# Kernel optimization log

Hardware: AMD Instinct MI355X
Metric: run time of the kernel (lower is better)

The kernel has to match this reference:

```python
import jax, jax.numpy as jnp
import numpy as np

D_MODEL = 1024


def pos_encoding(seq_len, d_model):
    # pos: [S,1], i: [d/2]
    pos = jnp.arange(seq_len, dtype=jnp.float32)[:, None]
    i = jnp.arange(0, d_model, 2, dtype=jnp.float32)
    angle_rates = 1.0 / jnp.power(10000.0, i / d_model)
    angle_rads = pos * angle_rates  # [S, d/2]
    # NOTE: original concatenates sin block then cos block (not interleaved)
    return jnp.concatenate([jnp.sin(angle_rads), jnp.cos(angle_rads)], axis=-1)  # [S, d]


def setup_inputs() -> dict:
    key = jax.random.key(0)
    ks = jax.random.split(key, 4)
    B, S, D = 4, 2048, D_MODEL
    scale = 1.0 / np.sqrt(D)
    x = jax.random.normal(ks[0], (B, S, D), dtype=jnp.float32)
    Wq = jax.random.normal(ks[1], (D, D), dtype=jnp.float32) * scale
    Wk = jax.random.normal(ks[2], (D, D), dtype=jnp.float32) * scale
    Wv = jax.random.normal(ks[3], (D, D), dtype=jnp.float32) * scale
    bq = jnp.zeros((D,), dtype=jnp.float32)
    bk = jnp.zeros((D,), dtype=jnp.float32)
    bv = jnp.zeros((D,), dtype=jnp.float32)
    return {"x": x, "Wq": Wq, "bq": bq, "Wk": Wk, "bk": bk, "Wv": Wv, "bv": bv}


def reference(x, Wq, bq, Wk, bk, Wv, bv):
    B, S, D = x.shape
    pe = pos_encoding(S, D)  # [S, D]
    h = x + pe[None, :, :]
    q = jnp.einsum('bsd,de->bse', h, Wq) + bq
    k = jnp.einsum('bsd,de->bse', h, Wk) + bk
    v = jnp.einsum('bsd,de->bse', h, Wv) + bv
    logits = jnp.einsum('bqd,bkd->bqk', q, k) / jnp.sqrt(jnp.float32(D))
    attn = jax.nn.softmax(logits, axis=-1)
    out = jnp.einsum('bqk,bkd->bqd', attn, v)
    return x + out
```

## Files before the change

kernel.cpp:

```cpp
#include <hip/hip_runtime.h>
#include <stdint.h>


#define AS1(p) ((__attribute__((address_space(1))) void*)(p))
#define AS3(p) ((__attribute__((address_space(3))) void*)(p))

typedef _Float16 f16x8 __attribute__((ext_vector_type(8)));
typedef _Float16 f16x4 __attribute__((ext_vector_type(4)));
typedef float f32x4 __attribute__((ext_vector_type(4)));

__global__ __launch_bounds__(256) void prep(const float* __restrict__ x,
                                            _Float16* __restrict__ h,
                                            const float* __restrict__ Wq,
                                            const float* __restrict__ Wk,
                                            const float* __restrict__ Wv,
                                            _Float16* __restrict__ Wt,
                                            float* __restrict__ rowsum) {
  const int bx = blockIdx.x;
  const int tid = threadIdx.x;
  if (bx < 8192) {
    const size_t e = ((size_t)bx * 256 + tid) * 4;
    const int d = (int)(e & 1023);
    const int s = (int)((e >> 10) & 2047);
    const float4 xv = *(const float4*)(x + e);
    const int half = d >> 9;
    const int j0 = d & 511;
    const float c = -0.017988946039016f;
    f16x4 o;
#pragma unroll
    for (int t = 0; t < 4; t++) {
      const float r = __expf((float)(j0 + t) * c);
      const float a = (float)s * r;
      const float p = half ? __cosf(a) : __sinf(a);
      const float xe = (t == 0) ? xv.x : (t == 1) ? xv.y : (t == 2) ? xv.z : xv.w;
      o[t] = (_Float16)(xe + p);
    }
    *(f16x4*)(h + e) = o;
  } else if (bx < 11264) {
    __shared__ float t[32][33];
    const int w = bx - 8192;
    const int z = w >> 10;
    const int rem = w & 1023;
    const int n0 = (rem & 31) * 32, k0 = (rem >> 5) * 32;
    const float* W = (z == 0) ? Wq : (z == 1) ? Wk : Wv;
    _Float16* o = Wt + (size_t)z * 1048576;
    const int tx = tid & 31, ty = tid >> 5;
#pragma unroll
    for (int i = ty; i < 32; i += 8)
      t[i][tx] = W[(size_t)(k0 + i) * 1024 + (n0 + tx)];
    __syncthreads();
#pragma unroll
    for (int i = ty; i < 32; i += 8)
      o[(size_t)(n0 + i) * 1024 + (k0 + tx)] = (_Float16)t[tx][i];
  } else {
    rowsum[(bx - 11264) * 256 + tid] = 0.f;
  }
}

template <int MODE, int NBUF>
__global__ __launch_bounds__(256) void gemm_bt(
    const _Float16* __restrict__ A0, long long sA,
    const _Float16* __restrict__ B0, long long sB,
    void* __restrict__ C0, long long sC,
    const float* __restrict__ aux0, const float* __restrict__ aux1,
    const float* __restrict__ aux2, float* __restrict__ rowsum,
    const _Float16* __restrict__ tin, _Float16* __restrict__ tout,
    long long sX, const int K, const int N, const int ldc) {
  __shared__ __align__(16) _Float16 As[NBUF * 128 * 32];
  __shared__ __align__(16) _Float16 Bs[NBUF * 128 * 32];
  const int tid = threadIdx.x;
  const int bid = blockIdx.x;

  if (MODE == 1 && bid >= 1024) {
    _Float16(*t)[33] = (_Float16(*)[33])As;
    const int w = bid - 1024;
    const int z = w >> 11;
    const int rem = w & 2047;
    const int d0 = (rem & 31) * 32, j0 = (rem >> 5) * 32;
    const _Float16* in = tin + (size_t)z * 2097152;
    _Float16* out = tout + (size_t)z * 2097152;
    const int tx = tid & 31, ty = tid >> 5;
#pragma unroll
    for (int i = ty; i < 32; i += 8)
      t[i][tx] = in[(size_t)(j0 + i) * 1024 + (d0 + tx)];
    __syncthreads();
#pragma unroll
    for (int i = ty; i < 32; i += 8)
      out[(size_t)(d0 + i) * 2048 + (j0 + tx)] = t[tx][i];
    return;
  }

  int z, bm0, bn0;
  if (MODE == 0) {
    const int c = bid & 7, t = bid >> 3;
    const int mhi = t & 7, u = t >> 3;
    bm0 = (mhi * 8 + c) * 128;
    bn0 = (u & 7) * 128;
    z = u >> 3;
  } else if (MODE == 1) {
    const int c = bid & 7, t = bid >> 3;
    const int zx = (t & 7) * 8 + c;
    const int y = t >> 3;
    z = zx >> 4; bm0 = (zx & 15) * 128; bn0 = y * 128;
  } else {
    const int c = bid & 7, t = bid >> 3;
    const int zx = (t & 3) * 8 + c;
    const int y = t >> 2;
    z = zx >> 3; bm0 = (zx & 7) * 128; bn0 = y * 128;
  }
  const _Float16* A = A0 + (size_t)z * sA;
  const _Float16* Bt = B0 + (size_t)z * sB;

  const _Float16* a0 = A + (size_t)(bm0 + (tid >> 2)) * K + (tid & 3) * 8;
  const _Float16* a1 = a0 + (size_t)64 * K;
  const _Float16* b0 = Bt + (size_t)(bn0 + (tid >> 2)) * K + (tid & 3) * 8;
  const _Float16* b1 = b0 + (size_t)64 * K;

  const int lane = tid & 63, wave = tid >> 6;
  const int wr = wave >> 1, wc = wave & 1;
  const int quad = lane >> 4, l16 = lane & 15;

  f32x4 acc[4][4];
#pragma unroll
  for (int i = 0; i < 4; i++)
#pragma unroll
    for (int j = 0; j < 4; j++) {
      f32x4 zz = {0.f, 0.f, 0.f, 0.f};
      acc[i][j] = zz;
    }

  for (int k0 = 0; k0 < K; k0 += 32 * NBUF) {
    __syncthreads();
#pragma unroll
    for (int u = 0; u < NBUF; u++) {
      __builtin_amdgcn_global_load_lds(AS1(a0 + k0 + u * 32),
                                       AS3(&As[u * 4096 + tid * 8]), 16, 0, 0);
      __builtin_amdgcn_global_load_lds(AS1(a1 + k0 + u * 32),
                                       AS3(&As[u * 4096 + tid * 8 + 2048]), 16, 0, 0);
      __builtin_amdgcn_global_load_lds(AS1(b0 + k0 + u * 32),
                                       AS3(&Bs[u * 4096 + tid * 8]), 16, 0, 0);
      __builtin_amdgcn_global_load_lds(AS1(b1 + k0 + u * 32),
                                       AS3(&Bs[u * 4096 + tid * 8 + 2048]), 16, 0, 0);
    }
    __syncthreads();
#pragma unroll
    for (int u = 0; u < NBUF; u++) {
      f16x8 af[4], bfr[4];
#pragma unroll
      for (int i = 0; i < 4; i++)
        af[i] = *(const f16x8*)&As[u * 4096 + (wr * 64 + i * 16 + l16) * 32 + quad * 8];
#pragma unroll
      for (int j = 0; j < 4; j++)
        bfr[j] = *(const f16x8*)&Bs[u * 4096 + (wc * 64 + j * 16 + l16) * 32 + quad * 8];
#pragma unroll
      for (int i = 0; i < 4; i++)
#pragma unroll
        for (int j = 0; j < 4; j++)
          acc[i][j] = __builtin_amdgcn_mfma_f32_16x16x32_f16(af[i], bfr[j],
                                                             acc[i][j], 0, 0, 0);
    }
  }

  const int rowb = bm0 + wr * 64 + quad * 4;
  const int colb = bn0 + wc * 64 + l16;
  if (MODE == 0) {
    _Float16* C = (_Float16*)C0 + (size_t)z * sC;
    const float* bias = (z == 0) ? aux0 : (z == 1) ? aux1 : aux2;
#pragma unroll
    for (int i = 0; i < 4; i++)
#pragma unroll
      for (int j = 0; j < 4; j++) {
        const int gn = colb + j * 16;
        const float bb = bias[gn];
#pragma unroll
        for (int r = 0; r < 4; r++)
          C[(size_t)(rowb + i * 16 + r) * N + gn] = (_Float16)(acc[i][j][r] + bb);
      }
  } else if (MODE == 1) {
    _Float16* C = (_Float16*)C0 + (size_t)z * sC;
    float rs[4] = {0.f, 0.f, 0.f, 0.f};
#pragma unroll
    for (int i = 0; i < 4; i++)
#pragma unroll
      for (int j = 0; j < 4; j++) {
        const int gn = colb + j * 16;
        f16x4 o;
        float pj = 0.f;
#pragma unroll
        for (int r = 0; r < 4; r++) {
          const float e = __expf(acc[i][j][r] * 0.03125f);
          o[r] = (_Float16)e;
          pj += e;
        }
        rs[j] += pj;
        *(f16x4*)&C[(size_t)gn * ldc + rowb + i * 16] = o;
      }
#pragma unroll
    for (int j = 0; j < 4; j++) {
      float v = rs[j];
      v += __shfl_xor(v, 16);
      v += __shfl_xor(v, 32);
      if (quad == 0) atomicAdd(&rowsum[z * 2048 + colb + j * 16], v);
    }
  } else {
    float* C = (float*)C0 + (size_t)z * sC;
    const float* X = aux0 + (size_t)z * sX;
    float inv[4];
#pragma unroll
    for (int j = 0; j < 4; j++)
      inv[j] = 1.0f / rowsum[z * 2048 + colb + j * 16];
#pragma unroll
    for (int i = 0; i < 4; i++)
#pragma unroll
      for (int j = 0; j < 4; j++) {
        const int gn = colb + j * 16;
        const size_t base = (size_t)gn * ldc + rowb + i * 16;
        const float4 xv = *(const float4*)(X + base);
        float4 o;
        o.x = acc[i][j][0] * inv[j] + xv.x;
        o.y = acc[i][j][1] * inv[j] + xv.y;
        o.z = acc[i][j][2] * inv[j] + xv.z;
        o.w = acc[i][j][3] * inv[j] + xv.w;
        *(float4*)(C + base) = o;
      }
  }
}

extern "C" void kernel_launch(void* const* d_in, const int* in_sizes, int n_in,
                              void* d_out, int out_size, void* d_ws, size_t ws_size,
                              hipStream_t stream) {
  (void)in_sizes; (void)n_in; (void)out_size; (void)ws_size;
  const float* x  = (const float*)d_in[0];
  const float* Wq = (const float*)d_in[1];
  const float* bq = (const float*)d_in[2];
  const float* Wk = (const float*)d_in[3];
  const float* bk = (const float*)d_in[4];
  const float* Wv = (const float*)d_in[5];
  const float* bv = (const float*)d_in[6];
  float* out = (float*)d_out;
  char* ws = (char*)d_ws;

  _Float16* h    = (_Float16*)(ws);
  _Float16* vT   = (_Float16*)(ws);
  _Float16* Wt   = (_Float16*)(ws + 16777216);
  _Float16* qkv  = (_Float16*)(ws + 23068672);
  _Float16* attn = (_Float16*)(ws + 73400320);
  float* rowsum  = (float*)   (ws + 106954752);

  const long long E = 8388608;

  prep<<<11296, 256, 0, stream>>>(x, h, Wq, Wk, Wv, Wt, rowsum);

  gemm_bt<0, 1><<<1536, 256, 0, stream>>>(
      h, 0LL, Wt, 1048576LL, qkv, E, bq, bk, bv, nullptr, nullptr, nullptr,
      0LL, 1024, 1024, 0);

  gemm_bt<1, 2><<<9216, 256, 0, stream>>>(
      qkv + E, 2097152LL, qkv, 2097152LL, attn, 4194304LL,
      nullptr, nullptr, nullptr, rowsum, qkv + 2 * E, vT,
      0LL, 1024, 2048, 2048);

  gemm_bt<2, 2><<<512, 256, 0, stream>>>(
      vT, 2097152LL, attn, 4194304LL, out, 2097152LL,
      x, nullptr, nullptr, rowsum, nullptr, nullptr,
      2097152LL, 2048, 2048, 1024);
}
```

Measured before the change: 292.7 us.

## Use 256x128 tiles with 512 threads and a 4-stage async LDS pipeline

The GEMM kernel moves from 128x128 tiles with 256 threads to 256x128 tiles with 512 threads and 8 waves. Blocks are remapped so launches use half as many blocks. A 4-deep ring of LDS buffers is filled by direct global-to-LDS loads issued three stages ahead, with explicit vmcnt waits and a single barrier per k-step, and s_setprio is raised around the MFMA block. The goal is to hide global load latency behind compute and cut barrier overhead. The cost is 96KB of LDS per block, which lowers occupancy, plus fragile hand-tuned waitcnt logic.

```diff
diff --git a/kernel.cpp b/kernel.cpp
--- a/kernel.cpp
+++ b/kernel.cpp
@@ -57,8 +57,8 @@
   }
 }
 
-template <int MODE, int NBUF>
-__global__ __launch_bounds__(256) void gemm_bt(
+template <int MODE>
+__global__ __launch_bounds__(512) void gemm_bt(
     const _Float16* __restrict__ A0, long long sA,
     const _Float16* __restrict__ B0, long long sB,
     void* __restrict__ C0, long long sC,
@@ -66,14 +66,14 @@
     const float* __restrict__ aux2, float* __restrict__ rowsum,
     const _Float16* __restrict__ tin, _Float16* __restrict__ tout,
     long long sX, const int K, const int N, const int ldc) {
-  __shared__ __align__(16) _Float16 As[NBUF * 128 * 32];
-  __shared__ __align__(16) _Float16 Bs[NBUF * 128 * 32];
+  __shared__ __align__(16) _Float16 As[4 * 8192];
+  __shared__ __align__(16) _Float16 Bs[4 * 4096];
   const int tid = threadIdx.x;
   const int bid = blockIdx.x;
 
-  if (MODE == 1 && bid >= 1024) {
-    _Float16(*t)[33] = (_Float16(*)[33])As;
-    const int w = bid - 1024;
+  if (MODE == 1 && bid >= 512) {
+    _Float16(*tb)[33] = (_Float16(*)[33])As;
+    const int w = bid - 512;
     const int z = w >> 11;
     const int rem = w & 2047;
     const int d0 = (rem & 31) * 32, j0 = (rem >> 5) * 32;
@@ -81,40 +81,47 @@
     _Float16* out = tout + (size_t)z * 2097152;
     const int tx = tid & 31, ty = tid >> 5;
 #pragma unroll
-    for (int i = ty; i < 32; i += 8)
-      t[i][tx] = in[(size_t)(j0 + i) * 1024 + (d0 + tx)];
+    for (int i = ty; i < 32; i += 16)
+      tb[i][tx] = in[(size_t)(j0 + i) * 1024 + (d0 + tx)];
     __syncthreads();
 #pragma unroll
-    for (int i = ty; i < 32; i += 8)
-      out[(size_t)(d0 + i) * 2048 + (j0 + tx)] = t[tx][i];
+    for (int i = ty; i < 32; i += 16)
+      out[(size_t)(d0 + i) * 2048 + (j0 + tx)] = tb[tx][i];
     return;
   }
 
   int z, bm0, bn0;
   if (MODE == 0) {
-    const int c = bid & 7, t = bid >> 3;
-    const int mhi = t & 7, u = t >> 3;
-    bm0 = (mhi * 8 + c) * 128;
-    bn0 = (u & 7) * 128;
-    z = u >> 3;
+    const int w = (bid & 7) * 96 + (bid >> 3);
+    const int m = w / 24, r = w - m * 24;
+    z = r >> 3; bm0 = m * 256; bn0 = (r & 7) * 128;
   } else if (MODE == 1) {
-    const int c = bid & 7, t = bid >> 3;
-    const int zx = (t & 7) * 8 + c;
-    const int y = t >> 3;
-    z = zx >> 4; bm0 = (zx & 15) * 128; bn0 = y * 128;
+    const int w = (bid & 7) * 64 + (bid >> 3);
+    z = w >> 7;
+    const int r = w & 127;
+    bm0 = (r >> 4) * 256; bn0 = (r & 15) * 128;
   } else {
-    const int c = bid & 7, t = bid >> 3;
-    const int zx = (t & 3) * 8 + c;
-    const int y = t >> 2;
-    z = zx >> 3; bm0 = (zx & 7) * 128; bn0 = y * 128;
+    const int w = (bid & 7) * 32 + (bid >> 3);
+    z = w >> 6;
+    const int r = w & 63;
+    bm0 = (r >> 4) * 256; bn0 = (r & 15) * 128;
   }
   const _Float16* A = A0 + (size_t)z * sA;
   const _Float16* Bt = B0 + (size_t)z * sB;
 
-  const _Float16* a0 = A + (size_t)(bm0 + (tid >> 2)) * K + (tid & 3) * 8;
-  const _Float16* a1 = a0 + (size_t)64 * K;
-  const _Float16* b0 = Bt + (size_t)(bn0 + (tid >> 2)) * K + (tid & 3) * 8;
-  const _Float16* b1 = b0 + (size_t)64 * K;
+  const _Float16* aS = A + (size_t)(bm0 + (tid >> 2)) * K + (tid & 3) * 8;
+  const _Float16* bS = Bt + (size_t)(bn0 + (tid >> 2)) * K + (tid & 3) * 8;
+  const size_t aHalf = (size_t)128 * K;
+
+  auto stage = [&](int kt) {
+    const int u = kt & 3;
+    const _Float16* ap = aS + kt * 32;
+    __builtin_amdgcn_global_load_lds(AS1(ap), AS3(&As[u * 8192 + tid * 8]), 16, 0, 0);
+    __builtin_amdgcn_global_load_lds(AS1(ap + aHalf),
+                                     AS3(&As[u * 8192 + 4096 + tid * 8]), 16, 0, 0);
+    __builtin_amdgcn_global_load_lds(AS1(bS + kt * 32),
+                                     AS3(&Bs[u * 4096 + tid * 8]), 16, 0, 0);
+  };
 
   const int lane = tid & 63, wave = tid >> 6;
   const int wr = wave >> 1, wc = wave & 1;
@@ -129,35 +136,37 @@
       acc[i][j] = zz;
     }
 
-  for (int k0 = 0; k0 < K; k0 += 32 * NBUF) {
-    __syncthreads();
-#pragma unroll
-    for (int u = 0; u < NBUF; u++) {
-      __builtin_amdgcn_global_load_lds(AS1(a0 + k0 + u * 32),
-                                       AS3(&As[u * 4096 + tid * 8]), 16, 0, 0);
-      __builtin_amdgcn_global_load_lds(AS1(a1 + k0 + u * 32),
-                                       AS3(&As[u * 4096 + tid * 8 + 2048]), 16, 0, 0);
-      __builtin_amdgcn_global_load_lds(AS1(b0 + k0 + u * 32),
-                                       AS3(&Bs[u * 4096 + tid * 8]), 16, 0, 0);
-      __builtin_amdgcn_global_load_lds(AS1(b1 + k0 + u * 32),
-                                       AS3(&Bs[u * 4096 + tid * 8 + 2048]), 16, 0, 0);
-    }
-    __syncthreads();
-#pragma unroll
-    for (int u = 0; u < NBUF; u++) {
-      f16x8 af[4], bfr[4];
-#pragma unroll
-      for (int i = 0; i < 4; i++)
-        af[i] = *(const f16x8*)&As[u * 4096 + (wr * 64 + i * 16 + l16) * 32 + quad * 8];
+  stage(0); stage(1); stage(2);
+  asm volatile("s_waitcnt vmcnt(6)" ::: "memory");
+  __builtin_amdgcn_s_barrier();
+  __builtin_amdgcn_sched_barrier(0);
+
+  const int nt = K >> 5;
+  for (int t = 0; t < nt; ++t) {
+    const int u = t & 3;
+    if (t + 3 < nt) stage(t + 3);
+    f16x8 af[4], bfr[4];
+#pragma unroll
+    for (int i = 0; i < 4; i++)
+      af[i] = *(const f16x8*)&As[u * 8192 + (wr * 64 + i * 16 + l16) * 32 + quad * 8];
+#pragma unroll
+    for (int j = 0; j < 4; j++)
+      bfr[j] = *(const f16x8*)&Bs[u * 4096 + (wc * 64 + j * 16 + l16) * 32 + quad * 8];
+    __builtin_amdgcn_s_setprio(1);
+#pragma unroll
+    for (int i = 0; i < 4; i++)
 #pragma unroll
       for (int j = 0; j < 4; j++)
-        bfr[j] = *(const f16x8*)&Bs[u * 4096 + (wc * 64 + j * 16 + l16) * 32 + quad * 8];
-#pragma unroll
-      for (int i = 0; i < 4; i++)
-#pragma unroll
-        for (int j = 0; j < 4; j++)
-          acc[i][j] = __builtin_amdgcn_mfma_f32_16x16x32_f16(af[i], bfr[j],
-                                                             acc[i][j], 0, 0, 0);
+        acc[i][j] = __builtin_amdgcn_mfma_f32_16x16x32_f16(af[i], bfr[j],
+                                                           acc[i][j], 0, 0, 0);
+    __builtin_amdgcn_s_setprio(0);
+    if (t + 1 < nt) {
+      __builtin_amdgcn_sched_barrier(0);
+      if (t + 3 < nt)        asm volatile("s_waitcnt vmcnt(6)" ::: "memory");
+      else if (t + 3 == nt)  asm volatile("s_waitcnt vmcnt(3)" ::: "memory");
+      else                   asm volatile("s_waitcnt vmcnt(0)" ::: "memory");
+      __builtin_amdgcn_s_barrier();
+      __builtin_amdgcn_sched_barrier(0);
     }
   }
 
@@ -251,16 +260,16 @@
 
   prep<<<11296, 256, 0, stream>>>(x, h, Wq, Wk, Wv, Wt, rowsum);
 
-  gemm_bt<0, 1><<<1536, 256, 0, stream>>>(
+  gemm_bt<0><<<768, 512, 0, stream>>>(
       h, 0LL, Wt, 1048576LL, qkv, E, bq, bk, bv, nullptr, nullptr, nullptr,
       0LL, 1024, 1024, 0);
 
-  gemm_bt<1, 2><<<9216, 256, 0, stream>>>(
+  gemm_bt<1><<<8704, 512, 0, stream>>>(
       qkv + E, 2097152LL, qkv, 2097152LL, attn, 4194304LL,
       nullptr, nullptr, nullptr, rowsum, qkv + 2 * E, vT,
       0LL, 1024, 2048, 2048);
 
-  gemm_bt<2, 2><<<512, 256, 0, stream>>>(
+  gemm_bt<2><<<256, 512, 0, stream>>>(
       vT, 2097152LL, attn, 4194304LL, out, 2097152LL,
       x, nullptr, nullptr, rowsum, nullptr, nullptr,
       2097152LL, 2048, 2048, 1024);
```

Measured after the change: 344.7 us. +17.8%, slower.
